# Optimization experiments

Hardware: AMD Instinct MI355X
Metric: run time of the kernel (lower is better)

Reference implementation:

```python
import jax, jax.numpy as jnp
import numpy as np

L, H, C, HS, E, K, V, BS = 2, 12, 768, 64, 8, 2, 32000, 1024
B, T = 2, 1024


def layer_norm(x, s, b):
    mu = x.mean(-1, keepdims=True)
    var = ((x - mu) ** 2).mean(-1, keepdims=True)
    return (x - mu) / jnp.sqrt(var + 1e-5) * s + b


def setup_inputs() -> dict:
    key = jax.random.key(0)
    ks = jax.random.split(key, 16)
    def n(k, shape, s=0.02):
        return jax.random.normal(k, shape, dtype=jnp.float32) * s
    return {
        'idx': jax.random.randint(ks[0], (B, T), 0, V),
        'targets': jax.random.randint(ks[1], (B, T), 0, V),
        'tok_emb': n(ks[2], (V, C)),
        'pos_emb': n(ks[3], (BS, C)),
        'ln1_s': jnp.ones((L, C), jnp.float32), 'ln1_b': jnp.zeros((L, C), jnp.float32),
        'wq': n(ks[4], (L, H, C, HS)), 'wk': n(ks[5], (L, H, C, HS)), 'wv': n(ks[6], (L, H, C, HS)),
        'wo': n(ks[7], (L, C, C)), 'bo': jnp.zeros((L, C), jnp.float32),
        'ln2_s': jnp.ones((L, C), jnp.float32), 'ln2_b': jnp.zeros((L, C), jnp.float32),
        'gate_w': n(ks[8], (L, E, C)),
        'w1': n(ks[9], (L, E, 4 * C, C)), 'b1': jnp.zeros((L, E, 4 * C), jnp.float32),
        'w2': n(ks[10], (L, E, C, 4 * C)), 'b2': jnp.zeros((L, E, C), jnp.float32),
        'lm_w': n(ks[11], (V, C)), 'lm_b': jnp.zeros((V,), jnp.float32),
    }


def reference(idx, targets, tok_emb, pos_emb, ln1_s, ln1_b, wq, wk, wv, wo, bo,
              ln2_s, ln2_b, gate_w, w1, b1, w2, b2, lm_w, lm_b):
    Bsz, Tn = idx.shape
    x = tok_emb[idx] + pos_emb[:Tn]                       # [B,T,C]
    mask = jnp.tril(jnp.ones((Tn, Tn), bool))
    for l in range(L):
        # causal multi-head attention (per-head projections, scale = n_embed**-0.5 as in source)
        h = layer_norm(x, ln1_s[l], ln1_b[l])
        q = jnp.einsum('btc,hcd->bhtd', h, wq[l])
        k = jnp.einsum('btc,hcd->bhtd', h, wk[l])
        v = jnp.einsum('btc,hcd->bhtd', h, wv[l])
        att = jnp.einsum('bhtd,bhsd->bhts', q, k) * (C ** -0.5)
        att = jax.nn.softmax(jnp.where(mask, att, -jnp.inf), axis=-1)
        o = jnp.einsum('bhts,bhsd->bhtd', att, v)
        o = o.transpose(0, 2, 1, 3).reshape(Bsz, Tn, C)   # concat heads
        x = x + jnp.einsum('btc,oc->bto', o, wo[l]) + bo[l]
        # MoE FFN: top-k routing, softmax over selected gate logits
        h2 = layer_norm(x, ln2_s[l], ln2_b[l]).reshape(-1, C)     # [N,C]
        gl = jnp.einsum('tc,ec->te', h2, gate_w[l])               # [N,E]
        wts, sel = jax.lax.top_k(gl, K)
        wts = jax.nn.softmax(wts, axis=-1)
        comb = jnp.einsum('tk,tke->te', wts, jax.nn.one_hot(sel, E, dtype=wts.dtype))
        hid = jax.nn.relu(jnp.einsum('tc,efc->etf', h2, w1[l]) + b1[l][:, None, :])
        y = jnp.einsum('etf,ecf->etc', hid, w2[l]) + b2[l][:, None, :]
        moe = jnp.einsum('te,etc->tc', comb, y)                   # dispatch-weighted combine
        x = x + moe.reshape(Bsz, Tn, C)
    logits = jnp.einsum('btc,vc->btv', x, lm_w) + lm_b
    lf = logits.reshape(-1, V)
    tf = targets.reshape(-1)
    loss = -jnp.take_along_axis(jax.nn.log_softmax(lf, axis=-1), tf[:, None], axis=1).mean()
    return lf, loss
```

## Files before the change

### kernel.cpp

```cpp
#include <hip/hip_runtime.h>
#include <hip/hip_bf16.h>

#define LCNT 2
#define HCNT 12
#define CDIM 768
#define HSD  64
#define ECNT 8
#define VOC  32000
#define BB   2
#define TT   1024
#define NTOK 2048
#define FF   3072
#define QKVLD 2304
#define TOTCAP 5120
#define SKN  4

typedef __attribute__((ext_vector_type(8))) short bf16x8;
typedef __attribute__((ext_vector_type(4))) float f32x4;

__device__ __forceinline__ float wave_sum(float v) {
    #pragma unroll
    for (int off = 32; off; off >>= 1) v += __shfl_xor(v, off);
    return v;
}
__device__ __forceinline__ float wave_max(float v) {
    #pragma unroll
    for (int off = 32; off; off >>= 1) v = fmaxf(v, __shfl_xor(v, off));
    return v;
}
__device__ __forceinline__ unsigned short f2bf(float f) {
    unsigned int u = __float_as_uint(f);
    unsigned int r = (u + 0x7FFFu + ((u >> 16) & 1u)) >> 16;
    return (unsigned short)r;
}
__device__ __forceinline__ float bf2f(unsigned short h) {
    return __uint_as_float((unsigned int)h << 16);
}
__device__ __forceinline__ void split2(float a, unsigned short& h, unsigned short& l) {
    h = f2bf(a);
    l = f2bf(a - bf2f(h));
}
__device__ __forceinline__ ushort4 cvt4(float4 v) {
    ushort4 r;
    r.x = f2bf(v.x); r.y = f2bf(v.y); r.z = f2bf(v.z); r.w = f2bf(v.w);
    return r;
}
__device__ __forceinline__ void gload16(const void* g, void* l) {
    __builtin_amdgcn_global_load_lds(
        (const __attribute__((address_space(1))) unsigned int*)g,
        (__attribute__((address_space(3))) unsigned int*)l,
        16, 0, 0);
}

__global__ __launch_bounds__(256)
void cvt_bf16_kernel(const float* __restrict__ in, unsigned short* __restrict__ out, int n4)
{
    for (int i = blockIdx.x * 256 + threadIdx.x; i < n4; i += gridDim.x * 256) {
        float4 v = reinterpret_cast<const float4*>(in)[i];
        reinterpret_cast<ushort4*>(out)[i] = cvt4(v);
    }
}

__global__ __launch_bounds__(256)
void splitw_kernel(const float* __restrict__ in, unsigned short* __restrict__ oh,
                   unsigned short* __restrict__ ol, int n4)
{
    for (int i = blockIdx.x * 256 + threadIdx.x; i < n4; i += gridDim.x * 256) {
        float4 v = reinterpret_cast<const float4*>(in)[i];
        ushort4 h, l;
        split2(v.x, h.x, l.x); split2(v.y, h.y, l.y);
        split2(v.z, h.z, l.z); split2(v.w, h.w, l.w);
        reinterpret_cast<ushort4*>(oh)[i] = h;
        reinterpret_cast<ushort4*>(ol)[i] = l;
    }
}

__global__ __launch_bounds__(256)
void embed_kernel(const int* __restrict__ idx, const float* __restrict__ tok,
                  const float* __restrict__ pos, float* __restrict__ x)
{
    int i = blockIdx.x * 256 + threadIdx.x;
    int c = i % CDIM;
    int n = i / CDIM;
    int t = n % TT;
    x[i] = tok[(size_t)idx[n] * CDIM + c] + pos[(size_t)t * CDIM + c];
}

__global__ __launch_bounds__(256)
void repack_kernel(const float* __restrict__ wq, const float* __restrict__ wk,
                   const float* __restrict__ wv, unsigned short* __restrict__ wph,
                   unsigned short* __restrict__ wpl)
{
    int i = blockIdx.x * 256 + threadIdx.x;
    int kk = i % CDIM;
    int n  = (i / CDIM) % CDIM;
    int w3 = (i / (CDIM * CDIM)) % 3;
    int l  = i / (CDIM * CDIM * 3);
    const float* src = (w3 == 0) ? wq : (w3 == 1) ? wk : wv;
    int h = n / HSD, d = n % HSD;
    float v = src[((((size_t)l * HCNT + h) * CDIM) + kk) * HSD + d];
    unsigned short hh, ll;
    split2(v, hh, ll);
    size_t o = (((size_t)l * 3 + w3) * CDIM + n) * CDIM + kk;
    wph[o] = hh;
    wpl[o] = ll;
}

__global__ __launch_bounds__(256)
void ln_kernel(const float* __restrict__ x, const float* __restrict__ sc,
               const float* __restrict__ bs, float* __restrict__ out)
{
    int row = blockIdx.x;
    const float* xr = x + (size_t)row * CDIM;
    float* orow = out + (size_t)row * CDIM;
    int tid = threadIdx.x;
    float v0 = xr[tid], v1 = xr[tid + 256], v2 = xr[tid + 512];
    float s1 = v0 + v1 + v2;
    float s2 = v0 * v0 + v1 * v1 + v2 * v2;
    s1 = wave_sum(s1);
    s2 = wave_sum(s2);
    __shared__ float r1[4], r2[4];
    int w = tid >> 6, lane = tid & 63;
    if (lane == 0) { r1[w] = s1; r2[w] = s2; }
    __syncthreads();
    float t1 = r1[0] + r1[1] + r1[2] + r1[3];
    float t2 = r2[0] + r2[1] + r2[2] + r2[3];
    float mu = t1 * (1.0f / CDIM);
    float var = t2 * (1.0f / CDIM) - mu * mu;
    float rstd = rsqrtf(var + 1e-5f);
    orow[tid]       = (v0 - mu) * rstd * sc[tid]       + bs[tid];
    orow[tid + 256] = (v1 - mu) * rstd * sc[tid + 256] + bs[tid + 256];
    orow[tid + 512] = (v2 - mu) * rstd * sc[tid + 512] + bs[tid + 512];
}

#define BM 128
#define BN 128
#define BK 32
#define PADK 40

template<int MODE, bool SPLIT>
__global__ __launch_bounds__(256)
void gemm_bf16_kernel(int Kd,
                      const float* __restrict__ A, int lda,
                      const float* __restrict__ B, int ldb,
                      const float* __restrict__ bias,
                      float* __restrict__ out, int ldo,
                      const int* __restrict__ rowmeta,
                      size_t bstride, int biasstride)
{
    __shared__ short Ah[BM * PADK];
    __shared__ short Bh[BN * PADK];
    __shared__ short Al[SPLIT ? BM * PADK : 2];
    __shared__ short Bl[SPLIT ? BN * PADK : 2];

    int roff = 0;
    if (rowmeta) {
        const int ee = blockIdx.z;
        const int rcnt = rowmeta[2 * ee + 1];
        if ((int)(blockIdx.y * BM) >= rcnt) return;
        roff = rowmeta[2 * ee];
        B += (size_t)ee * bstride;
        if (bias) bias += (size_t)ee * biasstride;
    }

    const int tid = threadIdx.x;
    const int m0 = roff + blockIdx.y * BM;
    const int n0 = blockIdx.x * BN;
    const int w = tid >> 6, lane = tid & 63;
    const int wr = w >> 1, wc = w & 1;
    const int lrow = lane & 15, lkg = lane >> 4;
    const int srow = tid >> 3, skg = (tid & 7) * 4;

    const float* Ablk = A + (size_t)m0 * lda;
    const float* Bblk = B + (size_t)n0 * ldb;

    float4 pa[4], pb[4];
    #pragma unroll
    for (int p = 0; p < 4; ++p) {
        pa[p] = *(const float4*)(Ablk + (size_t)(p * 32 + srow) * lda + skg);
        pb[p] = *(const float4*)(Bblk + (size_t)(p * 32 + srow) * ldb + skg);
    }

    f32x4 acc[4][4] = {};
    const int nk = Kd / BK;

    for (int t = 0; t < nk; ++t) {
        __syncthreads();
        #pragma unroll
        for (int p = 0; p < 4; ++p) {
            if constexpr (SPLIT) {
                ushort4 h, l;
                split2(pa[p].x, h.x, l.x); split2(pa[p].y, h.y, l.y);
                split2(pa[p].z, h.z, l.z); split2(pa[p].w, h.w, l.w);
                *(ushort4*)(&Ah[(p * 32 + srow) * PADK + skg]) = h;
                *(ushort4*)(&Al[(p * 32 + srow) * PADK + skg]) = l;
                split2(pb[p].x, h.x, l.x); split2(pb[p].y, h.y, l.y);
                split2(pb[p].z, h.z, l.z); split2(pb[p].w, h.w, l.w);
                *(ushort4*)(&Bh[(p * 32 + srow) * PADK + skg]) = h;
                *(ushort4*)(&Bl[(p * 32 + srow) * PADK + skg]) = l;
            } else {
                *(ushort4*)(&Ah[(p * 32 + srow) * PADK + skg]) = cvt4(pa[p]);
                *(ushort4*)(&Bh[(p * 32 + srow) * PADK + skg]) = cvt4(pb[p]);
            }
        }
        __syncthreads();
        if (t + 1 < nk) {
            const int kb = (t + 1) * BK + skg;
            #pragma unroll
            for (int p = 0; p < 4; ++p) {
                pa[p] = *(const float4*)(Ablk + (size_t)(p * 32 + srow) * lda + kb);
                pb[p] = *(const float4*)(Bblk + (size_t)(p * 32 + srow) * ldb + kb);
            }
        }
        bf16x8 afh[4], afl[4];
        #pragma unroll
        for (int i = 0; i < 4; ++i) {
            afh[i] = *(const bf16x8*)(&Ah[(wr * 64 + i * 16 + lrow) * PADK + lkg * 8]);
            if constexpr (SPLIT)
                afl[i] = *(const bf16x8*)(&Al[(wr * 64 + i * 16 + lrow) * PADK + lkg * 8]);
        }
        #pragma unroll
        for (int j = 0; j < 4; ++j) {
            const bf16x8 bh = *(const bf16x8*)(&Bh[(wc * 64 + j * 16 + lrow) * PADK + lkg * 8]);
            if constexpr (SPLIT) {
                const bf16x8 bl = *(const bf16x8*)(&Bl[(wc * 64 + j * 16 + lrow) * PADK + lkg * 8]);
                #pragma unroll
                for (int i = 0; i < 4; ++i) {
                    acc[i][j] = __builtin_amdgcn_mfma_f32_16x16x32_bf16(afh[i], bh, acc[i][j], 0, 0, 0);
                    acc[i][j] = __builtin_amdgcn_mfma_f32_16x16x32_bf16(afl[i], bh, acc[i][j], 0, 0, 0);
                    acc[i][j] = __builtin_amdgcn_mfma_f32_16x16x32_bf16(afh[i], bl, acc[i][j], 0, 0, 0);
                }
            } else {
                #pragma unroll
                for (int i = 0; i < 4; ++i)
                    acc[i][j] = __builtin_amdgcn_mfma_f32_16x16x32_bf16(afh[i], bh, acc[i][j], 0, 0, 0);
            }
        }
    }

    #pragma unroll
    for (int i = 0; i < 4; ++i) {
        #pragma unroll
        for (int r = 0; r < 4; ++r) {
            const int row = m0 + wr * 64 + i * 16 + lkg * 4 + r;
            #pragma unroll
            for (int j = 0; j < 4; ++j) {
                const int col = n0 + wc * 64 + j * 16 + lrow;
                const float bj = bias ? bias[col] : 0.0f;
                const float vres = acc[i][j][r] + bj;
                float* op = out + (size_t)row * ldo + col;
                if (MODE == 0) *op = vres;
                else if (MODE == 1) *op = *op + vres;
                else *op = fmaxf(vres, 0.0f);
            }
        }
    }
}

__global__ __launch_bounds__(256)
void gemm_sk_kernel(int Kc,
                    const float* __restrict__ A, int lda,
                    const float* __restrict__ B, int ldb,
                    const float* __restrict__ bias,
                    float* __restrict__ part, int ldo, size_t pstride,
                    const int* __restrict__ rowmeta,
                    size_t bstride, int biasstride)
{
    __shared__ short Ah[BM * PADK];
    __shared__ short Bh[BN * PADK];
    __shared__ short Al[BM * PADK];
    __shared__ short Bl[BN * PADK];

    const int zz = blockIdx.z;
    const int ee = zz / SKN, kz = zz % SKN;
    const int rcnt = rowmeta[2 * ee + 1];
    if ((int)(blockIdx.y * BM) >= rcnt) return;
    const int roff = rowmeta[2 * ee];
    const float* Bp = B + (size_t)ee * bstride + (size_t)kz * Kc;
    const float* Ap = A + (size_t)kz * Kc;
    const float* biasp = (kz == 0 && bias) ? bias + (size_t)ee * biasstride : nullptr;
    float* out = part + (size_t)kz * pstride;

    const int tid = threadIdx.x;
    const int m0 = roff + blockIdx.y * BM;
    const int n0 = blockIdx.x * BN;
    const int w = tid >> 6, lane = tid & 63;
    const int wr = w >> 1, wc = w & 1;
    const int lrow = lane & 15, lkg = lane >> 4;
    const int srow = tid >> 3, skg = (tid & 7) * 4;

    const float* Ablk = Ap + (size_t)m0 * lda;
    const float* Bblk = Bp + (size_t)n0 * ldb;

    float4 pa[4], pb[4];
    #pragma unroll
    for (int p = 0; p < 4; ++p) {
        pa[p] = *(const float4*)(Ablk + (size_t)(p * 32 + srow) * lda + skg);
        pb[p] = *(const float4*)(Bblk + (size_t)(p * 32 + srow) * ldb + skg);
    }

    f32x4 acc[4][4] = {};
    const int nk = Kc / BK;

    for (int t = 0; t < nk; ++t) {
        __syncthreads();
        #pragma unroll
        for (int p = 0; p < 4; ++p) {
            ushort4 h, l;
            split2(pa[p].x, h.x, l.x); split2(pa[p].y, h.y, l.y);
            split2(pa[p].z, h.z, l.z); split2(pa[p].w, h.w, l.w);
            *(ushort4*)(&Ah[(p * 32 + srow) * PADK + skg]) = h;
            *(ushort4*)(&Al[(p * 32 + srow) * PADK + skg]) = l;
            split2(pb[p].x, h.x, l.x); split2(pb[p].y, h.y, l.y);
            split2(pb[p].z, h.z, l.z); split2(pb[p].w, h.w, l.w);
            *(ushort4*)(&Bh[(p * 32 + srow) * PADK + skg]) = h;
            *(ushort4*)(&Bl[(p * 32 + srow) * PADK + skg]) = l;
        }
        __syncthreads();
        if (t + 1 < nk) {
            const int kb = (t + 1) * BK + skg;
            #pragma unroll
            for (int p = 0; p < 4; ++p) {
                pa[p] = *(const float4*)(Ablk + (size_t)(p * 32 + srow) * lda + kb);
                pb[p] = *(const float4*)(Bblk + (size_t)(p * 32 + srow) * ldb + kb);
            }
        }
        bf16x8 afh[4], afl[4];
        #pragma unroll
        for (int i = 0; i < 4; ++i) {
            afh[i] = *(const bf16x8*)(&Ah[(wr * 64 + i * 16 + lrow) * PADK + lkg * 8]);
            afl[i] = *(const bf16x8*)(&Al[(wr * 64 + i * 16 + lrow) * PADK + lkg * 8]);
        }
        #pragma unroll
        for (int j = 0; j < 4; ++j) {
            const bf16x8 bh = *(const bf16x8*)(&Bh[(wc * 64 + j * 16 + lrow) * PADK + lkg * 8]);
            const bf16x8 bl = *(const bf16x8*)(&Bl[(wc * 64 + j * 16 + lrow) * PADK + lkg * 8]);
            #pragma unroll
            for (int i = 0; i < 4; ++i) {
                acc[i][j] = __builtin_amdgcn_mfma_f32_16x16x32_bf16(afh[i], bh, acc[i][j], 0, 0, 0);
                acc[i][j] = __builtin_amdgcn_mfma_f32_16x16x32_bf16(afl[i], bh, acc[i][j], 0, 0, 0);
                acc[i][j] = __builtin_amdgcn_mfma_f32_16x16x32_bf16(afh[i], bl, acc[i][j], 0, 0, 0);
            }
        }
    }

    #pragma unroll
    for (int i = 0; i < 4; ++i) {
        #pragma unroll
        for (int r = 0; r < 4; ++r) {
            const int row = m0 + wr * 64 + i * 16 + lkg * 4 + r;
            #pragma unroll
            for (int j = 0; j < 4; ++j) {
                const int col = n0 + wc * 64 + j * 16 + lrow;
                const float bj = biasp ? biasp[col] : 0.0f;
                out[(size_t)row * ldo + col] = acc[i][j][r] + bj;
            }
        }
    }
}

template<int MODE, bool OUTSPLIT>
__global__ __launch_bounds__(256)
void gemm_splitpb_kernel(int Kd,
                         const float* __restrict__ A, int lda,
                         const unsigned short* __restrict__ Bhg,
                         const unsigned short* __restrict__ Blg, int ldb,
                         const float* __restrict__ bias,
                         float* __restrict__ out,
                         unsigned short* __restrict__ outh,
                         unsigned short* __restrict__ outl, int ldo)
{
    __shared__ short Ah[BM * PADK];
    __shared__ short Al[BM * PADK];
    __shared__ short Bh[BN * PADK];
    __shared__ short Bl[BN * PADK];

    const int tid = threadIdx.x;
    const int m0 = blockIdx.y * BM;
    const int n0 = blockIdx.x * BN;
    const int w = tid >> 6, lane = tid & 63;
    const int wr = w >> 1, wc = w & 1;
    const int lrow = lane & 15, lkg = lane >> 4;
    const int srow = tid >> 3, skg = (tid & 7) * 4;

    const float* Ablk = A + (size_t)m0 * lda;
    const unsigned short* Bhblk = Bhg + (size_t)n0 * ldb;
    const unsigned short* Blblk = Blg + (size_t)n0 * ldb;

    float4 pa[4];
    ushort4 pbh[4], pbl[4];
    #pragma unroll
    for (int p = 0; p < 4; ++p) {
        pa[p]  = *(const float4*)(Ablk + (size_t)(p * 32 + srow) * lda + skg);
        pbh[p] = *(const ushort4*)(Bhblk + (size_t)(p * 32 + srow) * ldb + skg);
        pbl[p] = *(const ushort4*)(Blblk + (size_t)(p * 32 + srow) * ldb + skg);
    }

    f32x4 acc[4][4] = {};
    const int nk = Kd / BK;

    for (int t = 0; t < nk; ++t) {
        __syncthreads();
        #pragma unroll
        for (int p = 0; p < 4; ++p) {
            ushort4 h, l;
            split2(pa[p].x, h.x, l.x); split2(pa[p].y, h.y, l.y);
            split2(pa[p].z, h.z, l.z); split2(pa[p].w, h.w, l.w);
            *(ushort4*)(&Ah[(p * 32 + srow) * PADK + skg]) = h;
            *(ushort4*)(&Al[(p * 32 + srow) * PADK + skg]) = l;
            *(ushort4*)(&Bh[(p * 32 + srow) * PADK + skg]) = pbh[p];
            *(ushort4*)(&Bl[(p * 32 + srow) * PADK + skg]) = pbl[p];
        }
        __syncthreads();
        if (t + 1 < nk) {
            const int kb = (t + 1) * BK + skg;
            #pragma unroll
            for (int p = 0; p < 4; ++p) {
                pa[p]  = *(const float4*)(Ablk + (size_t)(p * 32 + srow) * lda + kb);
                pbh[p] = *(const ushort4*)(Bhblk + (size_t)(p * 32 + srow) * ldb + kb);
                pbl[p] = *(const ushort4*)(Blblk + (size_t)(p * 32 + srow) * ldb + kb);
            }
        }
        bf16x8 afh[4], afl[4];
        #pragma unroll
        for (int i = 0; i < 4; ++i) {
            afh[i] = *(const bf16x8*)(&Ah[(wr * 64 + i * 16 + lrow) * PADK + lkg * 8]);
            afl[i] = *(const bf16x8*)(&Al[(wr * 64 + i * 16 + lrow) * PADK + lkg * 8]);
        }
        #pragma unroll
        for (int j = 0; j < 4; ++j) {
            const bf16x8 bh = *(const bf16x8*)(&Bh[(wc * 64 + j * 16 + lrow) * PADK + lkg * 8]);
            const bf16x8 bl = *(const bf16x8*)(&Bl[(wc * 64 + j * 16 + lrow) * PADK + lkg * 8]);
            #pragma unroll
            for (int i = 0; i < 4; ++i) {
                acc[i][j] = __builtin_amdgcn_mfma_f32_16x16x32_bf16(afh[i], bh, acc[i][j], 0, 0, 0);
                acc[i][j] = __builtin_amdgcn_mfma_f32_16x16x32_bf16(afl[i], bh, acc[i][j], 0, 0, 0);
                acc[i][j] = __builtin_amdgcn_mfma_f32_16x16x32_bf16(afh[i], bl, acc[i][j], 0, 0, 0);
            }
        }
    }

    #pragma unroll
    for (int i = 0; i < 4; ++i) {
        #pragma unroll
        for (int r = 0; r < 4; ++r) {
            const int row = m0 + wr * 64 + i * 16 + lkg * 4 + r;
            #pragma unroll
            for (int j = 0; j < 4; ++j) {
                const int col = n0 + wc * 64 + j * 16 + lrow;
                const float bj = bias ? bias[col] : 0.0f;
                const float vres = acc[i][j][r] + bj;
                if constexpr (OUTSPLIT) {
                    unsigned short h, l;
                    split2(vres, h, l);
                    outh[(size_t)row * ldo + col] = h;
                    outl[(size_t)row * ldo + col] = l;
                } else {
                    float* op = out + (size_t)row * ldo + col;
                    if (MODE == 0) *op = vres;
                    else *op = *op + vres;
                }
            }
        }
    }
}

template<int MODE, bool SWZ, bool OUTBF, bool BBF>
__global__ __launch_bounds__(256)
void gemm_fastw_kernel(int Kd,
                       const unsigned short* __restrict__ A, int lda,
                       const void* __restrict__ Bv, int ldb,
                       const float* __restrict__ bias,
                       void* __restrict__ outv, int ldo,
                       const int* __restrict__ rowmeta,
                       size_t bstride, int biasstride)
{
    __shared__ short Ah[BM * PADK];
    __shared__ short Bh[BN * PADK];

    int bx = blockIdx.x, by = blockIdx.y;
    if constexpr (SWZ) {
        const int nwg = gridDim.x * gridDim.y;
        const int chunk = nwg >> 3;
        const int flat = by * gridDim.x + bx;
        const int newid = (flat & 7) * chunk + (flat >> 3);
        by = newid % gridDim.y;
        bx = newid / gridDim.y;
    }

    const float* Bf = (const float*)Bv;
    const unsigned short* Bb = (const unsigned short*)Bv;
    float* outf = (float*)outv;
    unsigned short* outb = (unsigned short*)outv;

    int roff = 0;
    if (rowmeta) {
        const int ee = blockIdx.z;
        const int rcnt = rowmeta[2 * ee + 1];
        if ((int)(by * BM) >= rcnt) return;
        roff = rowmeta[2 * ee];
        if (BBF) Bb += (size_t)ee * bstride; else Bf += (size_t)ee * bstride;
        if (bias) bias += (size_t)ee * biasstride;
    }

    const int tid = threadIdx.x;
    const int m0 = roff + by * BM;
    const int n0 = bx * BN;
    const int w = tid >> 6, lane = tid & 63;
    const int wr = w >> 1, wc = w & 1;
    const int lrow = lane & 15, lkg = lane >> 4;
    const int srow = tid >> 3, skg = (tid & 7) * 4;

    const unsigned short* Ablk = A + (size_t)m0 * lda;
    const float* Bfblk = Bf + (size_t)n0 * ldb;
    const unsigned short* Bbblk = Bb + (size_t)n0 * ldb;

    ushort4 pa[4];
    ushort4 pbb[4];
    float4  pbf[4];
    #pragma unroll
    for (int p = 0; p < 4; ++p) {
        pa[p] = *(const ushort4*)(Ablk + (size_t)(p * 32 + srow) * lda + skg);
        if constexpr (BBF) pbb[p] = *(const ushort4*)(Bbblk + (size_t)(p * 32 + srow) * ldb + skg);
        else               pbf[p] = *(const float4*)(Bfblk + (size_t)(p * 32 + srow) * ldb + skg);
    }

    f32x4 acc[4][4] = {};
    const int nk = Kd / BK;

    for (int t = 0; t < nk; ++t) {
        __syncthreads();
        #pragma unroll
        for (int p = 0; p < 4; ++p) {
            *(ushort4*)(&Ah[(p * 32 + srow) * PADK + skg]) = pa[p];
            *(ushort4*)(&Bh[(p * 32 + srow) * PADK + skg]) = BBF ? pbb[p] : cvt4(pbf[p]);
        }
        __syncthreads();
        if (t + 1 < nk) {
            const int kb = (t + 1) * BK + skg;
            #pragma unroll
            for (int p = 0; p < 4; ++p) {
                pa[p] = *(const ushort4*)(Ablk + (size_t)(p * 32 + srow) * lda + kb);
                if constexpr (BBF) pbb[p] = *(const ushort4*)(Bbblk + (size_t)(p * 32 + srow) * ldb + kb);
                else               pbf[p] = *(const float4*)(Bfblk + (size_t)(p * 32 + srow) * ldb + kb);
            }
        }
        bf16x8 af[4];
        #pragma unroll
        for (int i = 0; i < 4; ++i)
            af[i] = *(const bf16x8*)(&Ah[(wr * 64 + i * 16 + lrow) * PADK + lkg * 8]);
        #pragma unroll
        for (int j = 0; j < 4; ++j) {
            const bf16x8 bh = *(const bf16x8*)(&Bh[(wc * 64 + j * 16 + lrow) * PADK + lkg * 8]);
            #pragma unroll
            for (int i = 0; i < 4; ++i)
                acc[i][j] = __builtin_amdgcn_mfma_f32_16x16x32_bf16(af[i], bh, acc[i][j], 0, 0, 0);
        }
    }

    #pragma unroll
    for (int i = 0; i < 4; ++i) {
        #pragma unroll
        for (int r = 0; r < 4; ++r) {
            const int row = m0 + wr * 64 + i * 16 + lkg * 4 + r;
            #pragma unroll
            for (int j = 0; j < 4; ++j) {
                const int col = n0 + wc * 64 + j * 16 + lrow;
                const float bj = bias ? bias[col] : 0.0f;
                float vres = acc[i][j][r] + bj;
                if (MODE == 2) vres = fmaxf(vres, 0.0f);
                if constexpr (OUTBF) outb[(size_t)row * ldo + col] = f2bf(vres);
                else                 outf[(size_t)row * ldo + col] = vres;
            }
        }
    }
}

template<bool SWZ>
__global__ __launch_bounds__(256)
void gemm_lds_kernel(int Kd,
                     const unsigned short* __restrict__ A, int lda,
                     const unsigned short* __restrict__ B, int ldb,
                     const float* __restrict__ bias,
                     float* __restrict__ out, int ldo)
{
    __shared__ unsigned short Asl[BM * BK];
    __shared__ unsigned short Bsl[BN * BK];

    int bx = blockIdx.x, by = blockIdx.y;
    if constexpr (SWZ) {
        const int nwg = gridDim.x * gridDim.y;
        const int chunk = nwg >> 3;
        const int flat = by * gridDim.x + bx;
        const int newid = (flat & 7) * chunk + (flat >> 3);
        by = newid % gridDim.y;
        bx = newid / gridDim.y;
    }

    const int tid = threadIdx.x;
    const int m0 = by * BM;
    const int n0 = bx * BN;
    const int w = tid >> 6, lane = tid & 63;
    const int wr = w >> 1, wc = w & 1;
    const int lrow = lane & 15, lkg = lane >> 4;
    const int grow = lane >> 2, gcol = (lane & 3) * 8;

    const unsigned short* Ablk = A + (size_t)m0 * lda;
    const unsigned short* Bblk = B + (size_t)n0 * ldb;

    f32x4 acc[4][4] = {};
    const int nk = Kd / BK;

    for (int t = 0; t < nk; ++t) {
        const int k0 = t * BK;
        __syncthreads();
        #pragma unroll
        for (int j = 0; j < 2; ++j) {
            const int rbase = w * 32 + j * 16;
            gload16(Ablk + (size_t)(rbase + grow) * lda + k0 + gcol, Asl + rbase * BK);
            gload16(Bblk + (size_t)(rbase + grow) * ldb + k0 + gcol, Bsl + rbase * BK);
        }
        __syncthreads();

        bf16x8 af[4];
        #pragma unroll
        for (int i = 0; i < 4; ++i)
            af[i] = *(const bf16x8*)(Asl + (wr * 64 + i * 16 + lrow) * BK + lkg * 8);
        #pragma unroll
        for (int j = 0; j < 4; ++j) {
            const bf16x8 bh = *(const bf16x8*)(Bsl + (wc * 64 + j * 16 + lrow) * BK + lkg * 8);
            #pragma unroll
            for (int i = 0; i < 4; ++i)
                acc[i][j] = __builtin_amdgcn_mfma_f32_16x16x32_bf16(af[i], bh, acc[i][j], 0, 0, 0);
        }
    }

    #pragma unroll
    for (int i = 0; i < 4; ++i) {
        #pragma unroll
        for (int r = 0; r < 4; ++r) {
            const int row = m0 + wr * 64 + i * 16 + lkg * 4 + r;
            #pragma unroll
            for (int j = 0; j < 4; ++j) {
                const int col = n0 + wc * 64 + j * 16 + lrow;
                const float bj = bias ? bias[col] : 0.0f;
                out[(size_t)row * ldo + col] = acc[i][j][r] + bj;
            }
        }
    }
}

#define QBLK 64
#define KVBLK 64

__global__ __launch_bounds__(256)
void attn_mfma_kernel(const unsigned short* __restrict__ qh_g,
                      const unsigned short* __restrict__ ql_g,
                      float* __restrict__ o)
{
    __shared__ short Kh[2][KVBLK][PADK];
    __shared__ short Kl[2][KVBLK][PADK];
    __shared__ short Vh[2][HSD][PADK];
    __shared__ short Vl[2][HSD][PADK];
    __shared__ short Ph[4][2][16][PADK];
    __shared__ short Pl[4][2][16][PADK];

    const int t0 = blockIdx.x * QBLK;
    const int bh = blockIdx.y;
    const int b = bh / HCNT, hh = bh % HCNT;
    const size_t baseq = (size_t)b * TT * QKVLD + (size_t)hh * HSD;
    const size_t obase = (size_t)b * TT * CDIM + (size_t)hh * HSD;
    const unsigned short* kh_g = qh_g + baseq + CDIM;
    const unsigned short* kl_g = ql_g + baseq + CDIM;
    const unsigned short* vh_g = qh_g + baseq + 2 * CDIM;
    const unsigned short* vl_g = ql_g + baseq + 2 * CDIM;
    const int tid = threadIdx.x;
    const int w = tid >> 6, lane = tid & 63;
    const int lrow = lane & 15, lkg = lane >> 4;
    const float sscale = rsqrtf((float)CDIM);

    bf16x8 qh[2], ql[2];
    {
        const size_t qroff = baseq + (size_t)(t0 + w * 16 + lrow) * QKVLD;
        #pragma unroll
        for (int ks = 0; ks < 2; ++ks) {
            qh[ks] = *(const bf16x8*)(qh_g + qroff + ks * 32 + lkg * 8);
            ql[ks] = *(const bf16x8*)(ql_g + qroff + ks * 32 + lkg * 8);
        }
    }

    f32x4 oacc[4] = {};
    float m_[4], l_[4];
    #pragma unroll
    for (int rr = 0; rr < 4; ++rr) { m_[rr] = -1e30f; l_[rr] = 0.0f; }

    for (int s0 = 0; s0 <= t0 + QBLK - 1; s0 += KVBLK) {
        __syncthreads();
        {
            const int srow = tid >> 3, skg = (tid & 7) * 4;
            #pragma unroll
            for (int p = 0; p < 2; ++p) {
                const size_t kroff = (size_t)(s0 + p * 32 + srow) * QKVLD;
                #pragma unroll
                for (int ks = 0; ks < 2; ++ks) {
                    *(ushort4*)(&Kh[ks][p * 32 + srow][skg]) = *(const ushort4*)(kh_g + kroff + ks * 32 + skg);
                    *(ushort4*)(&Kl[ks][p * 32 + srow][skg]) = *(const ushort4*)(kl_g + kroff + ks * 32 + skg);
                }
            }
            const int key = tid & 63, dg = (tid >> 6) * 16;
            const size_t vroff = (size_t)(s0 + key) * QKVLD + dg;
            const int kst = key >> 5, ko = key & 31;
            #pragma unroll
            for (int dd = 0; dd < 16; dd += 4) {
                ushort4 hv = *(const ushort4*)(vh_g + vroff + dd);
                ushort4 lv = *(const ushort4*)(vl_g + vroff + dd);
                Vh[kst][dg + dd + 0][ko] = hv.x; Vl[kst][dg + dd + 0][ko] = lv.x;
                Vh[kst][dg + dd + 1][ko] = hv.y; Vl[kst][dg + dd + 1][ko] = lv.y;
                Vh[kst][dg + dd + 2][ko] = hv.z; Vl[kst][dg + dd + 2][ko] = lv.z;
                Vh[kst][dg + dd + 3][ko] = hv.w; Vl[kst][dg + dd + 3][ko] = lv.w;
            }
        }
        __syncthreads();

        f32x4 sacc[4] = {};
        #pragma unroll
        for (int j = 0; j < 4; ++j) {
            #pragma unroll
            for (int ks = 0; ks < 2; ++ks) {
                const bf16x8 bh = *(const bf16x8*)(&Kh[ks][j * 16 + lrow][lkg * 8]);
                const bf16x8 bl = *(const bf16x8*)(&Kl[ks][j * 16 + lrow][lkg * 8]);
                sacc[j] = __builtin_amdgcn_mfma_f32_16x16x32_bf16(qh[ks], bh, sacc[j], 0, 0, 0);
                sacc[j] = __builtin_amdgcn_mfma_f32_16x16x32_bf16(ql[ks], bh, sacc[j], 0, 0, 0);
                sacc[j] = __builtin_amdgcn_mfma_f32_16x16x32_bf16(qh[ks], bl, sacc[j], 0, 0, 0);
            }
        }

        #pragma unroll
        for (int rr = 0; rr < 4; ++rr) {
            const int qi = t0 + w * 16 + lkg * 4 + rr;
            float pv[4];
            float mx = -1e30f;
            #pragma unroll
            for (int j = 0; j < 4; ++j) {
                float s = sacc[j][rr] * sscale;
                if (s0 + j * 16 + lrow > qi) s = -1e30f;
                pv[j] = s;
                mx = fmaxf(mx, s);
            }
            #pragma unroll
            for (int off = 1; off < 16; off <<= 1) mx = fmaxf(mx, __shfl_xor(mx, off));
            const float mnew = fmaxf(m_[rr], mx);
            const float corr = __expf(m_[rr] - mnew);
            float ps = 0.0f;
            #pragma unroll
            for (int j = 0; j < 4; ++j) { pv[j] = __expf(pv[j] - mnew); ps += pv[j]; }
            #pragma unroll
            for (int off = 1; off < 16; off <<= 1) ps += __shfl_xor(ps, off);
            l_[rr] = l_[rr] * corr + ps;
            m_[rr] = mnew;
            #pragma unroll
            for (int jd = 0; jd < 4; ++jd) oacc[jd][rr] *= corr;
            #pragma unroll
            for (int j = 0; j < 4; ++j) {
                unsigned short h, l;
                split2(pv[j], h, l);
                const int key = j * 16 + lrow;
                Ph[w][key >> 5][lkg * 4 + rr][key & 31] = h;
                Pl[w][key >> 5][lkg * 4 + rr][key & 31] = l;
            }
        }

        #pragma unroll
        for (int ks = 0; ks < 2; ++ks) {
            const bf16x8 ah = *(const bf16x8*)(&Ph[w][ks][lrow][lkg * 8]);
            const bf16x8 al = *(const bf16x8*)(&Pl[w][ks][lrow][lkg * 8]);
            #pragma unroll
            for (int jd = 0; jd < 4; ++jd) {
                const bf16x8 bh = *(const bf16x8*)(&Vh[ks][jd * 16 + lrow][lkg * 8]);
                const bf16x8 bl = *(const bf16x8*)(&Vl[ks][jd * 16 + lrow][lkg * 8]);
                oacc[jd] = __builtin_amdgcn_mfma_f32_16x16x32_bf16(ah, bh, oacc[jd], 0, 0, 0);
                oacc[jd] = __builtin_amdgcn_mfma_f32_16x16x32_bf16(al, bh, oacc[jd], 0, 0, 0);
                oacc[jd] = __builtin_amdgcn_mfma_f32_16x16x32_bf16(ah, bl, oacc[jd], 0, 0, 0);
            }
        }
    }

    #pragma unroll
    for (int rr = 0; rr < 4; ++rr) {
        const int qi = t0 + w * 16 + lkg * 4 + rr;
        const float invl = 1.0f / l_[rr];
        float* orow = o + obase + (size_t)qi * CDIM;
        #pragma unroll
        for (int jd = 0; jd < 4; ++jd)
            orow[jd * 16 + lrow] = oacc[jd][rr] * invl;
    }
}

__global__ __launch_bounds__(256)
void gate_kernel(const float* __restrict__ h2, const float* __restrict__ gw,
                 int2* __restrict__ sel, float2* __restrict__ wts)
{
    __shared__ float gws[ECNT * CDIM];
    int tid = threadIdx.x;
    for (int i = tid; i < ECNT * CDIM; i += 256) gws[i] = gw[i];
    __syncthreads();
    int t = blockIdx.x * 256 + tid;
    const float* hr = h2 + (size_t)t * CDIM;
    float g[ECNT] = {};
    for (int c = 0; c < CDIM; ++c) {
        float hv = hr[c];
        #pragma unroll
        for (int e = 0; e < ECNT; ++e) g[e] = fmaf(hv, gws[e * CDIM + c], g[e]);
    }
    int e0 = 0; float g0 = g[0];
    #pragma unroll
    for (int e = 1; e < ECNT; ++e) if (g[e] > g0) { g0 = g[e]; e0 = e; }
    int e1 = -1; float g1 = -1e30f;
    #pragma unroll
    for (int e = 0; e < ECNT; ++e) if (e != e0 && g[e] > g1) { g1 = g[e]; e1 = e; }
    float z = __expf(g1 - g0);
    float w0 = 1.0f / (1.0f + z);
    sel[t] = make_int2(e0, e1);
    wts[t] = make_float2(w0, 1.0f - w0);
}

__global__ __launch_bounds__(256)
void route_kernel(const int2* __restrict__ sel, int* __restrict__ perm,
                  int* __restrict__ tokpos, int* __restrict__ meta)
{
    __shared__ int cnt[ECNT], off[ECNT], cur[ECNT];
    const int tid = threadIdx.x;
    if (tid < ECNT) cnt[tid] = 0;
    __syncthreads();
    for (int t = tid; t < NTOK; t += 256) {
        atomicAdd(&cnt[sel[t].x], 1);
        atomicAdd(&cnt[sel[t].y], 1);
    }
    __syncthreads();
    if (tid == 0) {
        int run = 0;
        for (int e = 0; e < ECNT; ++e) {
            off[e] = run; cur[e] = 0;
            int pc = (cnt[e] + BM - 1) / BM * BM;
            meta[2 * e] = run; meta[2 * e + 1] = pc;
            run += pc;
        }
    }
    __syncthreads();
    for (int p = tid; p < TOTCAP; p += 256) perm[p] = 0;
    __syncthreads();
    for (int t = tid; t < NTOK; t += 256) {
        int2 s = sel[t];
        int p0 = atomicAdd(&cur[s.x], 1); perm[off[s.x] + p0] = t; tokpos[2 * t]     = off[s.x] + p0;
        int p1 = atomicAdd(&cur[s.y], 1); perm[off[s.y] + p1] = t; tokpos[2 * t + 1] = off[s.y] + p1;
    }
}

__global__ __launch_bounds__(256)
void gather_kernel(const float* __restrict__ h2, const int* __restrict__ perm,
                   float* __restrict__ xg)
{
    int i = blockIdx.x * 256 + threadIdx.x;
    int c = i % CDIM, p = i / CDIM;
    xg[i] = h2[(size_t)perm[p] * CDIM + c];
}

__global__ __launch_bounds__(256)
void gather_bf16_kernel(const float* __restrict__ h2, const int* __restrict__ perm,
                        unsigned short* __restrict__ xg)
{
    int i = blockIdx.x * 256 + threadIdx.x;
    int c = i % CDIM, p = i / CDIM;
    xg[i] = f2bf(h2[(size_t)perm[p] * CDIM + c]);
}

template<int SK>
__global__ __launch_bounds__(256)
void combine_kernel(const float* __restrict__ y, size_t pstride,
                    const int* __restrict__ tokpos,
                    const float2* __restrict__ wts, float* __restrict__ x)
{
    int i = blockIdx.x * 256 + threadIdx.x;
    int c = i % CDIM, t = i / CDIM;
    float2 wv = wts[t];
    const size_t r0 = (size_t)tokpos[2 * t] * CDIM + c;
    const size_t r1 = (size_t)tokpos[2 * t + 1] * CDIM + c;
    float a0 = 0.0f, a1 = 0.0f;
    #pragma unroll
    for (int s = 0; s < SK; ++s) {
        a0 += y[s * pstride + r0];
        a1 += y[s * pstride + r1];
    }
    x[i] += wv.x * a0 + wv.y * a1;
}

__global__ __launch_bounds__(256)
void loss_row_kernel(const float* __restrict__ logits, const int* __restrict__ tgt,
                     float* __restrict__ lrow)
{
    int row = blockIdx.x;
    const float* lr = logits + (size_t)row * VOC;
    int tid = threadIdx.x, w = tid >> 6, lane = tid & 63;
    __shared__ float red[4];
    float mx = -1e30f;
    for (int i = tid; i < VOC; i += 256) mx = fmaxf(mx, lr[i]);
    mx = wave_max(mx);
    if (lane == 0) red[w] = mx;
    __syncthreads();
    mx = fmaxf(fmaxf(red[0], red[1]), fmaxf(red[2], red[3]));
    __syncthreads();
    float se = 0.0f;
    for (int i = tid; i < VOC; i += 256) se += expf(lr[i] - mx);
    se = wave_sum(se);
    if (lane == 0) red[w] = se;
    __syncthreads();
    if (tid == 0) {
        float lse = mx + logf(red[0] + red[1] + red[2] + red[3]);
        lrow[row] = lse - lr[tgt[row]];
    }
}

__global__ __launch_bounds__(256)
void loss_reduce_kernel(const float* __restrict__ lrow, float* __restrict__ out)
{
    int tid = threadIdx.x, w = tid >> 6, lane = tid & 63;
    float s = 0.0f;
    for (int i = tid; i < NTOK; i += 256) s += lrow[i];
    s = wave_sum(s);
    __shared__ float red[4];
    if (lane == 0) red[w] = s;
    __syncthreads();
    if (tid == 0) out[0] = (red[0] + red[1] + red[2] + red[3]) * (1.0f / NTOK);
}

extern "C" void kernel_launch(void* const* d_in, const int* in_sizes, int n_in,
                              void* d_out, int out_size, void* d_ws, size_t ws_size,
                              hipStream_t stream)
{
    const int*   idx     = (const int*)d_in[0];
    const int*   targets = (const int*)d_in[1];
    const float* tok_emb = (const float*)d_in[2];
    const float* pos_emb = (const float*)d_in[3];
    const float* ln1_s   = (const float*)d_in[4];
    const float* ln1_b   = (const float*)d_in[5];
    const float* wq      = (const float*)d_in[6];
    const float* wk      = (const float*)d_in[7];
    const float* wv      = (const float*)d_in[8];
    const float* wo      = (const float*)d_in[9];
    const float* bo      = (const float*)d_in[10];
    const float* ln2_s   = (const float*)d_in[11];
    const float* ln2_b   = (const float*)d_in[12];
    const float* gate_w  = (const float*)d_in[13];
    const float* w1      = (const float*)d_in[14];
    const float* b1      = (const float*)d_in[15];
    const float* w2      = (const float*)d_in[16];
    const float* b2      = (const float*)d_in[17];
    const float* lm_w    = (const float*)d_in[18];
    const float* lm_b    = (const float*)d_in[19];
    float* out = (float*)d_out;

    unsigned short* wph = (unsigned short*)d_ws;
    unsigned short* wpl = wph + (size_t)3 * LCNT * CDIM * CDIM;
    unsigned short* woh = wpl + (size_t)3 * LCNT * CDIM * CDIM;
    unsigned short* wol = woh + (size_t)LCNT * CDIM * CDIM;
    float* x    = (float*)(wol + (size_t)LCNT * CDIM * CDIM);
    float* hbuf = x    + (size_t)NTOK * CDIM;
    float* qkv  = hbuf + (size_t)NTOK * CDIM;
    float* xg   = qkv  + (size_t)NTOK * QKVLD;
    float* hid  = xg   + (size_t)TOTCAP * CDIM;
    float* lrow = hid  + (size_t)TOTCAP * FF;
    float2* wts = (float2*)(lrow + NTOK);
    int2*  sel  = (int2*)(wts + NTOK);
    int*   perm = (int*)(sel + NTOK);
    int*  tokpos= perm + TOTCAP;
    int*   meta = tokpos + 2 * NTOK;
    unsigned short* x_bf = (unsigned short*)(meta + 16);
    float* part = (float*)(x_bf + (size_t)NTOK * CDIM);

    const size_t need_bytes = (size_t)((char*)(part + (size_t)SKN * TOTCAP * CDIM) - (char*)d_ws);
    const bool use_sk = ws_size >= need_bytes;

    unsigned short* qkvh = (unsigned short*)qkv;
    unsigned short* qkvl = qkvh + (size_t)NTOK * QKVLD;
    unsigned short* xg_bf  = (unsigned short*)xg;
    unsigned short* hid_bf = (unsigned short*)hid;
    unsigned short* lmw_bf = (unsigned short*)hid;

    dim3 blk(256);

    repack_kernel<<<(3 * LCNT * CDIM * CDIM) / 256, blk, 0, stream>>>(wq, wk, wv, wph, wpl);
    splitw_kernel<<<1024, blk, 0, stream>>>(wo, woh, wol, LCNT * CDIM * CDIM / 4);
    embed_kernel<<<(NTOK * CDIM) / 256, blk, 0, stream>>>(idx, tok_emb, pos_emb, x);

    for (int l = 0; l < LCNT; ++l) {
        ln_kernel<<<NTOK, blk, 0, stream>>>(x, ln1_s + (size_t)l * CDIM, ln1_b + (size_t)l * CDIM, hbuf);

        gemm_splitpb_kernel<0, true><<<dim3(QKVLD / BN, NTOK / BM), blk, 0, stream>>>(
            CDIM, hbuf, CDIM, wph + (size_t)l * 3 * CDIM * CDIM, wpl + (size_t)l * 3 * CDIM * CDIM,
            CDIM, nullptr, nullptr, qkvh, qkvl, QKVLD);

        attn_mfma_kernel<<<dim3(TT / QBLK, BB * HCNT), blk, 0, stream>>>(qkvh, qkvl, hbuf);

        gemm_splitpb_kernel<1, false><<<dim3(CDIM / BN, NTOK / BM), blk, 0, stream>>>(
            CDIM, hbuf, CDIM, woh + (size_t)l * CDIM * CDIM, wol + (size_t)l * CDIM * CDIM,
            CDIM, bo + (size_t)l * CDIM, x, nullptr, nullptr, CDIM);

        float* h2 = qkv;
        float* ybuf = qkv;
        ln_kernel<<<NTOK, blk, 0, stream>>>(x, ln2_s + (size_t)l * CDIM, ln2_b + (size_t)l * CDIM, h2);
        gate_kernel<<<NTOK / 256, blk, 0, stream>>>(h2, gate_w + (size_t)l * ECNT * CDIM, sel, wts);
        route_kernel<<<1, blk, 0, stream>>>(sel, perm, tokpos, meta);

        const float* w1l = w1 + (size_t)l * ECNT * FF * CDIM;
        const float* b1l = b1 + (size_t)l * ECNT * FF;
        const float* w2l = w2 + (size_t)l * ECNT * CDIM * FF;
        const float* b2l = b2 + (size_t)l * ECNT * CDIM;
        if (l == 0) {
            gather_kernel<<<(TOTCAP * CDIM) / 256, blk, 0, stream>>>(h2, perm, xg);
            gemm_bf16_kernel<2, true><<<dim3(FF / BN, TOTCAP / BM, ECNT), blk, 0, stream>>>(
                CDIM, xg, CDIM, w1l, CDIM, b1l, hid, FF, meta, (size_t)FF * CDIM, FF);
            if (use_sk) {
                gemm_sk_kernel<<<dim3(CDIM / BN, TOTCAP / BM, ECNT * SKN), blk, 0, stream>>>(
                    FF / SKN, hid, FF, w2l, FF, b2l, part, CDIM, (size_t)TOTCAP * CDIM,
                    meta, (size_t)CDIM * FF, CDIM);
                combine_kernel<SKN><<<(NTOK * CDIM) / 256, blk, 0, stream>>>(
                    part, (size_t)TOTCAP * CDIM, tokpos, wts, x);
            } else {
                gemm_bf16_kernel<0, true><<<dim3(CDIM / BN, TOTCAP / BM, ECNT), blk, 0, stream>>>(
                    FF, hid, FF, w2l, FF, b2l, ybuf, CDIM, meta, (size_t)CDIM * FF, CDIM);
                combine_kernel<1><<<(NTOK * CDIM) / 256, blk, 0, stream>>>(
                    ybuf, 0, tokpos, wts, x);
            }
        } else {
            gather_bf16_kernel<<<(TOTCAP * CDIM) / 256, blk, 0, stream>>>(h2, perm, xg_bf);
            gemm_fastw_kernel<2, false, true, false><<<dim3(FF / BN, TOTCAP / BM, ECNT), blk, 0, stream>>>(
                CDIM, xg_bf, CDIM, w1l, CDIM, b1l, hid_bf, FF, meta, (size_t)FF * CDIM, FF);
            gemm_fastw_kernel<0, false, false, false><<<dim3(CDIM / BN, TOTCAP / BM, ECNT), blk, 0, stream>>>(
                FF, hid_bf, FF, w2l, FF, b2l, ybuf, CDIM, meta, (size_t)CDIM * FF, CDIM);
            combine_kernel<1><<<(NTOK * CDIM) / 256, blk, 0, stream>>>(
                ybuf, 0, tokpos, wts, x);
        }
    }

    cvt_bf16_kernel<<<2048, blk, 0, stream>>>(lm_w, lmw_bf, VOC * CDIM / 4);
    cvt_bf16_kernel<<<512, blk, 0, stream>>>(x, x_bf, NTOK * CDIM / 4);

    gemm_lds_kernel<true><<<dim3(VOC / BN, NTOK / BM), blk, 0, stream>>>(
        CDIM, x_bf, CDIM, lmw_bf, CDIM, lm_b, out, VOC);

    loss_row_kernel<<<NTOK, blk, 0, stream>>>(out, targets, lrow);
    loss_reduce_kernel<<<1, blk, 0, stream>>>(lrow, out + (size_t)NTOK * VOC);
}
```

Before: 1.372 ms.

## Pre-split activations into bf16 hi/lo pairs at producers instead of in GEMMs

LayerNorm, attention output and the first MoE GEMM now write activations as separate bf16 high/low halves. Consumer GEMMs load those halves directly instead of loading fp32 and splitting each tile inside the K loop. This removes repeated split arithmetic and halves nothing in bytes (hi+lo equals fp32 size), but moves the conversion out of the hot loop and lets gathers copy shorts. The loss row kernel is also vectorised with float4 loads.

```diff
diff --git a/kernel.cpp b/kernel.cpp
--- a/kernel.cpp
+++ b/kernel.cpp
@@ -106,13 +106,14 @@
     wpl[o] = ll;
 }
 
+template<bool WF32>
 __global__ __launch_bounds__(256)
 void ln_kernel(const float* __restrict__ x, const float* __restrict__ sc,
-               const float* __restrict__ bs, float* __restrict__ out)
+               const float* __restrict__ bs, float* __restrict__ out,
+               unsigned short* __restrict__ oh, unsigned short* __restrict__ ol)
 {
     int row = blockIdx.x;
     const float* xr = x + (size_t)row * CDIM;
-    float* orow = out + (size_t)row * CDIM;
     int tid = threadIdx.x;
     float v0 = xr[tid], v1 = xr[tid + 256], v2 = xr[tid + 512];
     float s1 = v0 + v1 + v2;
@@ -128,9 +129,19 @@
     float mu = t1 * (1.0f / CDIM);
     float var = t2 * (1.0f / CDIM) - mu * mu;
     float rstd = rsqrtf(var + 1e-5f);
-    orow[tid]       = (v0 - mu) * rstd * sc[tid]       + bs[tid];
-    orow[tid + 256] = (v1 - mu) * rstd * sc[tid + 256] + bs[tid + 256];
-    orow[tid + 512] = (v2 - mu) * rstd * sc[tid + 512] + bs[tid + 512];
+    float o0 = (v0 - mu) * rstd * sc[tid]       + bs[tid];
+    float o1 = (v1 - mu) * rstd * sc[tid + 256] + bs[tid + 256];
+    float o2 = (v2 - mu) * rstd * sc[tid + 512] + bs[tid + 512];
+    if constexpr (WF32) {
+        float* orow = out + (size_t)row * CDIM;
+        orow[tid] = o0; orow[tid + 256] = o1; orow[tid + 512] = o2;
+    }
+    unsigned short h, l;
+    unsigned short* ohr = oh + (size_t)row * CDIM;
+    unsigned short* olr = ol + (size_t)row * CDIM;
+    split2(o0, h, l); ohr[tid]       = h; olr[tid]       = l;
+    split2(o1, h, l); ohr[tid + 256] = h; olr[tid + 256] = l;
+    split2(o2, h, l); ohr[tid + 512] = h; olr[tid + 512] = l;
 }
 
 #define BM 128
@@ -138,237 +149,17 @@
 #define BK 32
 #define PADK 40
 
-template<int MODE, bool SPLIT>
-__global__ __launch_bounds__(256)
-void gemm_bf16_kernel(int Kd,
-                      const float* __restrict__ A, int lda,
-                      const float* __restrict__ B, int ldb,
-                      const float* __restrict__ bias,
-                      float* __restrict__ out, int ldo,
-                      const int* __restrict__ rowmeta,
-                      size_t bstride, int biasstride)
-{
-    __shared__ short Ah[BM * PADK];
-    __shared__ short Bh[BN * PADK];
-    __shared__ short Al[SPLIT ? BM * PADK : 2];
-    __shared__ short Bl[SPLIT ? BN * PADK : 2];
-
-    int roff = 0;
-    if (rowmeta) {
-        const int ee = blockIdx.z;
-        const int rcnt = rowmeta[2 * ee + 1];
-        if ((int)(blockIdx.y * BM) >= rcnt) return;
-        roff = rowmeta[2 * ee];
-        B += (size_t)ee * bstride;
-        if (bias) bias += (size_t)ee * biasstride;
-    }
-
-    const int tid = threadIdx.x;
-    const int m0 = roff + blockIdx.y * BM;
-    const int n0 = blockIdx.x * BN;
-    const int w = tid >> 6, lane = tid & 63;
-    const int wr = w >> 1, wc = w & 1;
-    const int lrow = lane & 15, lkg = lane >> 4;
-    const int srow = tid >> 3, skg = (tid & 7) * 4;
-
-    const float* Ablk = A + (size_t)m0 * lda;
-    const float* Bblk = B + (size_t)n0 * ldb;
-
-    float4 pa[4], pb[4];
-    #pragma unroll
-    for (int p = 0; p < 4; ++p) {
-        pa[p] = *(const float4*)(Ablk + (size_t)(p * 32 + srow) * lda + skg);
-        pb[p] = *(const float4*)(Bblk + (size_t)(p * 32 + srow) * ldb + skg);
-    }
-
-    f32x4 acc[4][4] = {};
-    const int nk = Kd / BK;
-
-    for (int t = 0; t < nk; ++t) {
-        __syncthreads();
-        #pragma unroll
-        for (int p = 0; p < 4; ++p) {
-            if constexpr (SPLIT) {
-                ushort4 h, l;
-                split2(pa[p].x, h.x, l.x); split2(pa[p].y, h.y, l.y);
-                split2(pa[p].z, h.z, l.z); split2(pa[p].w, h.w, l.w);
-                *(ushort4*)(&Ah[(p * 32 + srow) * PADK + skg]) = h;
-                *(ushort4*)(&Al[(p * 32 + srow) * PADK + skg]) = l;
-                split2(pb[p].x, h.x, l.x); split2(pb[p].y, h.y, l.y);
-                split2(pb[p].z, h.z, l.z); split2(pb[p].w, h.w, l.w);
-                *(ushort4*)(&Bh[(p * 32 + srow) * PADK + skg]) = h;
-                *(ushort4*)(&Bl[(p * 32 + srow) * PADK + skg]) = l;
-            } else {
-                *(ushort4*)(&Ah[(p * 32 + srow) * PADK + skg]) = cvt4(pa[p]);
-                *(ushort4*)(&Bh[(p * 32 + srow) * PADK + skg]) = cvt4(pb[p]);
-            }
-        }
-        __syncthreads();
-        if (t + 1 < nk) {
-            const int kb = (t + 1) * BK + skg;
-            #pragma unroll
-            for (int p = 0; p < 4; ++p) {
-                pa[p] = *(const float4*)(Ablk + (size_t)(p * 32 + srow) * lda + kb);
-                pb[p] = *(const float4*)(Bblk + (size_t)(p * 32 + srow) * ldb + kb);
-            }
-        }
-        bf16x8 afh[4], afl[4];
-        #pragma unroll
-        for (int i = 0; i < 4; ++i) {
-            afh[i] = *(const bf16x8*)(&Ah[(wr * 64 + i * 16 + lrow) * PADK + lkg * 8]);
-            if constexpr (SPLIT)
-                afl[i] = *(const bf16x8*)(&Al[(wr * 64 + i * 16 + lrow) * PADK + lkg * 8]);
-        }
-        #pragma unroll
-        for (int j = 0; j < 4; ++j) {
-            const bf16x8 bh = *(const bf16x8*)(&Bh[(wc * 64 + j * 16 + lrow) * PADK + lkg * 8]);
-            if constexpr (SPLIT) {
-                const bf16x8 bl = *(const bf16x8*)(&Bl[(wc * 64 + j * 16 + lrow) * PADK + lkg * 8]);
-                #pragma unroll
-                for (int i = 0; i < 4; ++i) {
-                    acc[i][j] = __builtin_amdgcn_mfma_f32_16x16x32_bf16(afh[i], bh, acc[i][j], 0, 0, 0);
-                    acc[i][j] = __builtin_amdgcn_mfma_f32_16x16x32_bf16(afl[i], bh, acc[i][j], 0, 0, 0);
-                    acc[i][j] = __builtin_amdgcn_mfma_f32_16x16x32_bf16(afh[i], bl, acc[i][j], 0, 0, 0);
-                }
-            } else {
-                #pragma unroll
-                for (int i = 0; i < 4; ++i)
-                    acc[i][j] = __builtin_amdgcn_mfma_f32_16x16x32_bf16(afh[i], bh, acc[i][j], 0, 0, 0);
-            }
-        }
-    }
-
-    #pragma unroll
-    for (int i = 0; i < 4; ++i) {
-        #pragma unroll
-        for (int r = 0; r < 4; ++r) {
-            const int row = m0 + wr * 64 + i * 16 + lkg * 4 + r;
-            #pragma unroll
-            for (int j = 0; j < 4; ++j) {
-                const int col = n0 + wc * 64 + j * 16 + lrow;
-                const float bj = bias ? bias[col] : 0.0f;
-                const float vres = acc[i][j][r] + bj;
-                float* op = out + (size_t)row * ldo + col;
-                if (MODE == 0) *op = vres;
-                else if (MODE == 1) *op = *op + vres;
-                else *op = fmaxf(vres, 0.0f);
-            }
-        }
-    }
-}
-
-__global__ __launch_bounds__(256)
-void gemm_sk_kernel(int Kc,
-                    const float* __restrict__ A, int lda,
-                    const float* __restrict__ B, int ldb,
+template<int MODE, bool OUTSPLIT>
+__global__ __launch_bounds__(256)
+void gemm_ps_kernel(int Kd,
+                    const unsigned short* __restrict__ Ahg,
+                    const unsigned short* __restrict__ Alg, int lda,
+                    const unsigned short* __restrict__ Bhg,
+                    const unsigned short* __restrict__ Blg, int ldb,
                     const float* __restrict__ bias,
-                    float* __restrict__ part, int ldo, size_t pstride,
-                    const int* __restrict__ rowmeta,
-                    size_t bstride, int biasstride)
-{
-    __shared__ short Ah[BM * PADK];
-    __shared__ short Bh[BN * PADK];
-    __shared__ short Al[BM * PADK];
-    __shared__ short Bl[BN * PADK];
-
-    const int zz = blockIdx.z;
-    const int ee = zz / SKN, kz = zz % SKN;
-    const int rcnt = rowmeta[2 * ee + 1];
-    if ((int)(blockIdx.y * BM) >= rcnt) return;
-    const int roff = rowmeta[2 * ee];
-    const float* Bp = B + (size_t)ee * bstride + (size_t)kz * Kc;
-    const float* Ap = A + (size_t)kz * Kc;
-    const float* biasp = (kz == 0 && bias) ? bias + (size_t)ee * biasstride : nullptr;
-    float* out = part + (size_t)kz * pstride;
-
-    const int tid = threadIdx.x;
-    const int m0 = roff + blockIdx.y * BM;
-    const int n0 = blockIdx.x * BN;
-    const int w = tid >> 6, lane = tid & 63;
-    const int wr = w >> 1, wc = w & 1;
-    const int lrow = lane & 15, lkg = lane >> 4;
-    const int srow = tid >> 3, skg = (tid & 7) * 4;
-
-    const float* Ablk = Ap + (size_t)m0 * lda;
-    const float* Bblk = Bp + (size_t)n0 * ldb;
-
-    float4 pa[4], pb[4];
-    #pragma unroll
-    for (int p = 0; p < 4; ++p) {
-        pa[p] = *(const float4*)(Ablk + (size_t)(p * 32 + srow) * lda + skg);
-        pb[p] = *(const float4*)(Bblk + (size_t)(p * 32 + srow) * ldb + skg);
-    }
-
-    f32x4 acc[4][4] = {};
-    const int nk = Kc / BK;
-
-    for (int t = 0; t < nk; ++t) {
-        __syncthreads();
-        #pragma unroll
-        for (int p = 0; p < 4; ++p) {
-            ushort4 h, l;
-            split2(pa[p].x, h.x, l.x); split2(pa[p].y, h.y, l.y);
-            split2(pa[p].z, h.z, l.z); split2(pa[p].w, h.w, l.w);
-            *(ushort4*)(&Ah[(p * 32 + srow) * PADK + skg]) = h;
-            *(ushort4*)(&Al[(p * 32 + srow) * PADK + skg]) = l;
-            split2(pb[p].x, h.x, l.x); split2(pb[p].y, h.y, l.y);
-            split2(pb[p].z, h.z, l.z); split2(pb[p].w, h.w, l.w);
-            *(ushort4*)(&Bh[(p * 32 + srow) * PADK + skg]) = h;
-            *(ushort4*)(&Bl[(p * 32 + srow) * PADK + skg]) = l;
-        }
-        __syncthreads();
-        if (t + 1 < nk) {
-            const int kb = (t + 1) * BK + skg;
-            #pragma unroll
-            for (int p = 0; p < 4; ++p) {
-                pa[p] = *(const float4*)(Ablk + (size_t)(p * 32 + srow) * lda + kb);
-                pb[p] = *(const float4*)(Bblk + (size_t)(p * 32 + srow) * ldb + kb);
-            }
-        }
-        bf16x8 afh[4], afl[4];
-        #pragma unroll
-        for (int i = 0; i < 4; ++i) {
-            afh[i] = *(const bf16x8*)(&Ah[(wr * 64 + i * 16 + lrow) * PADK + lkg * 8]);
-            afl[i] = *(const bf16x8*)(&Al[(wr * 64 + i * 16 + lrow) * PADK + lkg * 8]);
-        }
-        #pragma unroll
-        for (int j = 0; j < 4; ++j) {
-            const bf16x8 bh = *(const bf16x8*)(&Bh[(wc * 64 + j * 16 + lrow) * PADK + lkg * 8]);
-            const bf16x8 bl = *(const bf16x8*)(&Bl[(wc * 64 + j * 16 + lrow) * PADK + lkg * 8]);
-            #pragma unroll
-            for (int i = 0; i < 4; ++i) {
-                acc[i][j] = __builtin_amdgcn_mfma_f32_16x16x32_bf16(afh[i], bh, acc[i][j], 0, 0, 0);
-                acc[i][j] = __builtin_amdgcn_mfma_f32_16x16x32_bf16(afl[i], bh, acc[i][j], 0, 0, 0);
-                acc[i][j] = __builtin_amdgcn_mfma_f32_16x16x32_bf16(afh[i], bl, acc[i][j], 0, 0, 0);
-            }
-        }
-    }
-
-    #pragma unroll
-    for (int i = 0; i < 4; ++i) {
-        #pragma unroll
-        for (int r = 0; r < 4; ++r) {
-            const int row = m0 + wr * 64 + i * 16 + lkg * 4 + r;
-            #pragma unroll
-            for (int j = 0; j < 4; ++j) {
-                const int col = n0 + wc * 64 + j * 16 + lrow;
-                const float bj = biasp ? biasp[col] : 0.0f;
-                out[(size_t)row * ldo + col] = acc[i][j][r] + bj;
-            }
-        }
-    }
-}
-
-template<int MODE, bool OUTSPLIT>
-__global__ __launch_bounds__(256)
-void gemm_splitpb_kernel(int Kd,
-                         const float* __restrict__ A, int lda,
-                         const unsigned short* __restrict__ Bhg,
-                         const unsigned short* __restrict__ Blg, int ldb,
-                         const float* __restrict__ bias,
-                         float* __restrict__ out,
-                         unsigned short* __restrict__ outh,
-                         unsigned short* __restrict__ outl, int ldo)
+                    float* __restrict__ out,
+                    unsigned short* __restrict__ outh,
+                    unsigned short* __restrict__ outl, int ldo)
 {
     __shared__ short Ah[BM * PADK];
     __shared__ short Al[BM * PADK];
@@ -383,17 +174,18 @@
     const int lrow = lane & 15, lkg = lane >> 4;
     const int srow = tid >> 3, skg = (tid & 7) * 4;
 
-    const float* Ablk = A + (size_t)m0 * lda;
-    const unsigned short* Bhblk = Bhg + (size_t)n0 * ldb;
-    const unsigned short* Blblk = Blg + (size_t)n0 * ldb;
-
-    float4 pa[4];
-    ushort4 pbh[4], pbl[4];
+    const unsigned short* Ahb = Ahg + (size_t)m0 * lda;
+    const unsigned short* Alb = Alg + (size_t)m0 * lda;
+    const unsigned short* Bhb = Bhg + (size_t)n0 * ldb;
+    const unsigned short* Blb = Blg + (size_t)n0 * ldb;
+
+    ushort4 pah[4], pal[4], pbh[4], pbl[4];
     #pragma unroll
     for (int p = 0; p < 4; ++p) {
-        pa[p]  = *(const float4*)(Ablk + (size_t)(p * 32 + srow) * lda + skg);
-        pbh[p] = *(const ushort4*)(Bhblk + (size_t)(p * 32 + srow) * ldb + skg);
-        pbl[p] = *(const ushort4*)(Blblk + (size_t)(p * 32 + srow) * ldb + skg);
+        pah[p] = *(const ushort4*)(Ahb + (size_t)(p * 32 + srow) * lda + skg);
+        pal[p] = *(const ushort4*)(Alb + (size_t)(p * 32 + srow) * lda + skg);
+        pbh[p] = *(const ushort4*)(Bhb + (size_t)(p * 32 + srow) * ldb + skg);
+        pbl[p] = *(const ushort4*)(Blb + (size_t)(p * 32 + srow) * ldb + skg);
     }
 
     f32x4 acc[4][4] = {};
@@ -403,11 +195,8 @@
         __syncthreads();
         #pragma unroll
         for (int p = 0; p < 4; ++p) {
-            ushort4 h, l;
-            split2(pa[p].x, h.x, l.x); split2(pa[p].y, h.y, l.y);
-            split2(pa[p].z, h.z, l.z); split2(pa[p].w, h.w, l.w);
-            *(ushort4*)(&Ah[(p * 32 + srow) * PADK + skg]) = h;
-            *(ushort4*)(&Al[(p * 32 + srow) * PADK + skg]) = l;
+            *(ushort4*)(&Ah[(p * 32 + srow) * PADK + skg]) = pah[p];
+            *(ushort4*)(&Al[(p * 32 + srow) * PADK + skg]) = pal[p];
             *(ushort4*)(&Bh[(p * 32 + srow) * PADK + skg]) = pbh[p];
             *(ushort4*)(&Bl[(p * 32 + srow) * PADK + skg]) = pbl[p];
         }
@@ -416,9 +205,10 @@
             const int kb = (t + 1) * BK + skg;
             #pragma unroll
             for (int p = 0; p < 4; ++p) {
-                pa[p]  = *(const float4*)(Ablk + (size_t)(p * 32 + srow) * lda + kb);
-                pbh[p] = *(const ushort4*)(Bhblk + (size_t)(p * 32 + srow) * ldb + kb);
-                pbl[p] = *(const ushort4*)(Blblk + (size_t)(p * 32 + srow) * ldb + kb);
+                pah[p] = *(const ushort4*)(Ahb + (size_t)(p * 32 + srow) * lda + kb);
+                pal[p] = *(const ushort4*)(Alb + (size_t)(p * 32 + srow) * lda + kb);
+                pbh[p] = *(const ushort4*)(Bhb + (size_t)(p * 32 + srow) * ldb + kb);
+                pbl[p] = *(const ushort4*)(Blb + (size_t)(p * 32 + srow) * ldb + kb);
             }
         }
         bf16x8 afh[4], afl[4];
@@ -465,6 +255,219 @@
     }
 }
 
+__global__ __launch_bounds__(256)
+void gemm_pse_kernel(int Kd,
+                     const unsigned short* __restrict__ Ahg,
+                     const unsigned short* __restrict__ Alg, int lda,
+                     const float* __restrict__ B, int ldb,
+                     const float* __restrict__ bias,
+                     unsigned short* __restrict__ outh,
+                     unsigned short* __restrict__ outl, int ldo,
+                     const int* __restrict__ rowmeta,
+                     size_t bstride, int biasstride)
+{
+    __shared__ short Ah[BM * PADK];
+    __shared__ short Al[BM * PADK];
+    __shared__ short Bh[BN * PADK];
+    __shared__ short Bl[BN * PADK];
+
+    const int ee = blockIdx.z;
+    const int rcnt = rowmeta[2 * ee + 1];
+    if ((int)(blockIdx.y * BM) >= rcnt) return;
+    const int roff = rowmeta[2 * ee];
+    B += (size_t)ee * bstride;
+    bias += (size_t)ee * biasstride;
+
+    const int tid = threadIdx.x;
+    const int m0 = roff + blockIdx.y * BM;
+    const int n0 = blockIdx.x * BN;
+    const int w = tid >> 6, lane = tid & 63;
+    const int wr = w >> 1, wc = w & 1;
+    const int lrow = lane & 15, lkg = lane >> 4;
+    const int srow = tid >> 3, skg = (tid & 7) * 4;
+
+    const unsigned short* Ahb = Ahg + (size_t)m0 * lda;
+    const unsigned short* Alb = Alg + (size_t)m0 * lda;
+    const float* Bblk = B + (size_t)n0 * ldb;
+
+    ushort4 pah[4], pal[4];
+    float4 pb[4];
+    #pragma unroll
+    for (int p = 0; p < 4; ++p) {
+        pah[p] = *(const ushort4*)(Ahb + (size_t)(p * 32 + srow) * lda + skg);
+        pal[p] = *(const ushort4*)(Alb + (size_t)(p * 32 + srow) * lda + skg);
+        pb[p]  = *(const float4*)(Bblk + (size_t)(p * 32 + srow) * ldb + skg);
+    }
+
+    f32x4 acc[4][4] = {};
+    const int nk = Kd / BK;
+
+    for (int t = 0; t < nk; ++t) {
+        __syncthreads();
+        #pragma unroll
+        for (int p = 0; p < 4; ++p) {
+            *(ushort4*)(&Ah[(p * 32 + srow) * PADK + skg]) = pah[p];
+            *(ushort4*)(&Al[(p * 32 + srow) * PADK + skg]) = pal[p];
+            ushort4 h, l;
+            split2(pb[p].x, h.x, l.x); split2(pb[p].y, h.y, l.y);
+            split2(pb[p].z, h.z, l.z); split2(pb[p].w, h.w, l.w);
+            *(ushort4*)(&Bh[(p * 32 + srow) * PADK + skg]) = h;
+            *(ushort4*)(&Bl[(p * 32 + srow) * PADK + skg]) = l;
+        }
+        __syncthreads();
+        if (t + 1 < nk) {
+            const int kb = (t + 1) * BK + skg;
+            #pragma unroll
+            for (int p = 0; p < 4; ++p) {
+                pah[p] = *(const ushort4*)(Ahb + (size_t)(p * 32 + srow) * lda + kb);
+                pal[p] = *(const ushort4*)(Alb + (size_t)(p * 32 + srow) * lda + kb);
+                pb[p]  = *(const float4*)(Bblk + (size_t)(p * 32 + srow) * ldb + kb);
+            }
+        }
+        bf16x8 afh[4], afl[4];
+        #pragma unroll
+        for (int i = 0; i < 4; ++i) {
+            afh[i] = *(const bf16x8*)(&Ah[(wr * 64 + i * 16 + lrow) * PADK + lkg * 8]);
+            afl[i] = *(const bf16x8*)(&Al[(wr * 64 + i * 16 + lrow) * PADK + lkg * 8]);
+        }
+        #pragma unroll
+        for (int j = 0; j < 4; ++j) {
+            const bf16x8 bh = *(const bf16x8*)(&Bh[(wc * 64 + j * 16 + lrow) * PADK + lkg * 8]);
+            const bf16x8 bl = *(const bf16x8*)(&Bl[(wc * 64 + j * 16 + lrow) * PADK + lkg * 8]);
+            #pragma unroll
+            for (int i = 0; i < 4; ++i) {
+                acc[i][j] = __builtin_amdgcn_mfma_f32_16x16x32_bf16(afh[i], bh, acc[i][j], 0, 0, 0);
+                acc[i][j] = __builtin_amdgcn_mfma_f32_16x16x32_bf16(afl[i], bh, acc[i][j], 0, 0, 0);
+                acc[i][j] = __builtin_amdgcn_mfma_f32_16x16x32_bf16(afh[i], bl, acc[i][j], 0, 0, 0);
+            }
+        }
+    }
+
+    #pragma unroll
+    for (int i = 0; i < 4; ++i) {
+        #pragma unroll
+        for (int r = 0; r < 4; ++r) {
+            const int row = m0 + wr * 64 + i * 16 + lkg * 4 + r;
+            #pragma unroll
+            for (int j = 0; j < 4; ++j) {
+                const int col = n0 + wc * 64 + j * 16 + lrow;
+                const float vres = fmaxf(acc[i][j][r] + bias[col], 0.0f);
+                unsigned short h, l;
+                split2(vres, h, l);
+                outh[(size_t)row * ldo + col] = h;
+                outl[(size_t)row * ldo + col] = l;
+            }
+        }
+    }
+}
+
+template<int SK>
+__global__ __launch_bounds__(256)
+void gemm_pssk_kernel(int Kc,
+                      const unsigned short* __restrict__ Ahg,
+                      const unsigned short* __restrict__ Alg, int lda,
+                      const float* __restrict__ B, int ldb,
+                      const float* __restrict__ bias,
+                      float* __restrict__ part, int ldo, size_t pstride,
+                      const int* __restrict__ rowmeta,
+                      size_t bstride, int biasstride)
+{
+    __shared__ short Ah[BM * PADK];
+    __shared__ short Al[BM * PADK];
+    __shared__ short Bh[BN * PADK];
+    __shared__ short Bl[BN * PADK];
+
+    const int zz = blockIdx.z;
+    const int ee = zz / SK, kz = zz % SK;
+    const int rcnt = rowmeta[2 * ee + 1];
+    if ((int)(blockIdx.y * BM) >= rcnt) return;
+    const int roff = rowmeta[2 * ee];
+    const float* Bp = B + (size_t)ee * bstride + (size_t)kz * Kc;
+    const unsigned short* Ahp = Ahg + (size_t)kz * Kc;
+    const unsigned short* Alp = Alg + (size_t)kz * Kc;
+    const float* biasp = (kz == 0) ? bias + (size_t)ee * biasstride : nullptr;
+    float* out = part + (size_t)kz * pstride;
+
+    const int tid = threadIdx.x;
+    const int m0 = roff + blockIdx.y * BM;
+    const int n0 = blockIdx.x * BN;
+    const int w = tid >> 6, lane = tid & 63;
+    const int wr = w >> 1, wc = w & 1;
+    const int lrow = lane & 15, lkg = lane >> 4;
+    const int srow = tid >> 3, skg = (tid & 7) * 4;
+
+    const unsigned short* Ahb = Ahp + (size_t)m0 * lda;
+    const unsigned short* Alb = Alp + (size_t)m0 * lda;
+    const float* Bblk = Bp + (size_t)n0 * ldb;
+
+    ushort4 pah[4], pal[4];
+    float4 pb[4];
+    #pragma unroll
+    for (int p = 0; p < 4; ++p) {
+        pah[p] = *(const ushort4*)(Ahb + (size_t)(p * 32 + srow) * lda + skg);
+        pal[p] = *(const ushort4*)(Alb + (size_t)(p * 32 + srow) * lda + skg);
+        pb[p]  = *(const float4*)(Bblk + (size_t)(p * 32 + srow) * ldb + skg);
+    }
+
+    f32x4 acc[4][4] = {};
+    const int nk = Kc / BK;
+
+    for (int t = 0; t < nk; ++t) {
+        __syncthreads();
+        #pragma unroll
+        for (int p = 0; p < 4; ++p) {
+            *(ushort4*)(&Ah[(p * 32 + srow) * PADK + skg]) = pah[p];
+            *(ushort4*)(&Al[(p * 32 + srow) * PADK + skg]) = pal[p];
+            ushort4 h, l;
+            split2(pb[p].x, h.x, l.x); split2(pb[p].y, h.y, l.y);
+            split2(pb[p].z, h.z, l.z); split2(pb[p].w, h.w, l.w);
+            *(ushort4*)(&Bh[(p * 32 + srow) * PADK + skg]) = h;
+            *(ushort4*)(&Bl[(p * 32 + srow) * PADK + skg]) = l;
+        }
+        __syncthreads();
+        if (t + 1 < nk) {
+            const int kb = (t + 1) * BK + skg;
+            #pragma unroll
+            for (int p = 0; p < 4; ++p) {
+                pah[p] = *(const ushort4*)(Ahb + (size_t)(p * 32 + srow) * lda + kb);
+                pal[p] = *(const ushort4*)(Alb + (size_t)(p * 32 + srow) * lda + kb);
+                pb[p]  = *(const float4*)(Bblk + (size_t)(p * 32 + srow) * ldb + kb);
+            }
+        }
+        bf16x8 afh[4], afl[4];
+        #pragma unroll
+        for (int i = 0; i < 4; ++i) {
+            afh[i] = *(const bf16x8*)(&Ah[(wr * 64 + i * 16 + lrow) * PADK + lkg * 8]);
+            afl[i] = *(const bf16x8*)(&Al[(wr * 64 + i * 16 + lrow) * PADK + lkg * 8]);
+        }
+        #pragma unroll
+        for (int j = 0; j < 4; ++j) {
+            const bf16x8 bh = *(const bf16x8*)(&Bh[(wc * 64 + j * 16 + lrow) * PADK + lkg * 8]);
+            const bf16x8 bl = *(const bf16x8*)(&Bl[(wc * 64 + j * 16 + lrow) * PADK + lkg * 8]);
+            #pragma unroll
+            for (int i = 0; i < 4; ++i) {
+                acc[i][j] = __builtin_amdgcn_mfma_f32_16x16x32_bf16(afh[i], bh, acc[i][j], 0, 0, 0);
+                acc[i][j] = __builtin_amdgcn_mfma_f32_16x16x32_bf16(afl[i], bh, acc[i][j], 0, 0, 0);
+                acc[i][j] = __builtin_amdgcn_mfma_f32_16x16x32_bf16(afh[i], bl, acc[i][j], 0, 0, 0);
+            }
+        }
+    }
+
+    #pragma unroll
+    for (int i = 0; i < 4; ++i) {
+        #pragma unroll
+        for (int r = 0; r < 4; ++r) {
+            const int row = m0 + wr * 64 + i * 16 + lkg * 4 + r;
+            #pragma unroll
+            for (int j = 0; j < 4; ++j) {
+                const int col = n0 + wc * 64 + j * 16 + lrow;
+                const float bj = biasp ? biasp[col] : 0.0f;
+                out[(size_t)row * ldo + col] = acc[i][j][r] + bj;
+            }
+        }
+    }
+}
+
 template<int MODE, bool SWZ, bool OUTBF, bool BBF>
 __global__ __launch_bounds__(256)
 void gemm_fastw_kernel(int Kd,
@@ -656,7 +659,8 @@
 __global__ __launch_bounds__(256)
 void attn_mfma_kernel(const unsigned short* __restrict__ qh_g,
                       const unsigned short* __restrict__ ql_g,
-                      float* __restrict__ o)
+                      unsigned short* __restrict__ oh_g,
+                      unsigned short* __restrict__ ol_g)
 {
     __shared__ short Kh[2][KVBLK][PADK];
     __shared__ short Kl[2][KVBLK][PADK];
@@ -789,10 +793,14 @@
     for (int rr = 0; rr < 4; ++rr) {
         const int qi = t0 + w * 16 + lkg * 4 + rr;
         const float invl = 1.0f / l_[rr];
-        float* orow = o + obase + (size_t)qi * CDIM;
-        #pragma unroll
-        for (int jd = 0; jd < 4; ++jd)
-            orow[jd * 16 + lrow] = oacc[jd][rr] * invl;
+        const size_t orow = obase + (size_t)qi * CDIM;
+        #pragma unroll
+        for (int jd = 0; jd < 4; ++jd) {
+            unsigned short h, l;
+            split2(oacc[jd][rr] * invl, h, l);
+            oh_g[orow + jd * 16 + lrow] = h;
+            ol_g[orow + jd * 16 + lrow] = l;
+        }
     }
 }
 
@@ -857,21 +865,26 @@
 }
 
 __global__ __launch_bounds__(256)
-void gather_kernel(const float* __restrict__ h2, const int* __restrict__ perm,
-                   float* __restrict__ xg)
+void gather_ps_kernel(const unsigned short* __restrict__ h2h,
+                      const unsigned short* __restrict__ h2l,
+                      const int* __restrict__ perm,
+                      unsigned short* __restrict__ xgh,
+                      unsigned short* __restrict__ xgl)
 {
     int i = blockIdx.x * 256 + threadIdx.x;
     int c = i % CDIM, p = i / CDIM;
-    xg[i] = h2[(size_t)perm[p] * CDIM + c];
-}
-
-__global__ __launch_bounds__(256)
-void gather_bf16_kernel(const float* __restrict__ h2, const int* __restrict__ perm,
-                        unsigned short* __restrict__ xg)
+    const size_t s = (size_t)perm[p] * CDIM + c;
+    xgh[i] = h2h[s];
+    xgl[i] = h2l[s];
+}
+
+__global__ __launch_bounds__(256)
+void gather_cp_kernel(const unsigned short* __restrict__ h2h, const int* __restrict__ perm,
+                      unsigned short* __restrict__ xg)
 {
     int i = blockIdx.x * 256 + threadIdx.x;
     int c = i % CDIM, p = i / CDIM;
-    xg[i] = f2bf(h2[(size_t)perm[p] * CDIM + c]);
+    xg[i] = h2h[(size_t)perm[p] * CDIM + c];
 }
 
 template<int SK>
@@ -899,24 +912,30 @@
                      float* __restrict__ lrow)
 {
     int row = blockIdx.x;
-    const float* lr = logits + (size_t)row * VOC;
+    const float4* lr4 = (const float4*)(logits + (size_t)row * VOC);
     int tid = threadIdx.x, w = tid >> 6, lane = tid & 63;
     __shared__ float red[4];
     float mx = -1e30f;
-    for (int i = tid; i < VOC; i += 256) mx = fmaxf(mx, lr[i]);
+    for (int i = tid; i < VOC / 4; i += 256) {
+        float4 v = lr4[i];
+        mx = fmaxf(mx, fmaxf(fmaxf(v.x, v.y), fmaxf(v.z, v.w)));
+    }
     mx = wave_max(mx);
     if (lane == 0) red[w] = mx;
     __syncthreads();
     mx = fmaxf(fmaxf(red[0], red[1]), fmaxf(red[2], red[3]));
     __syncthreads();
     float se = 0.0f;
-    for (int i = tid; i < VOC; i += 256) se += expf(lr[i] - mx);
+    for (int i = tid; i < VOC / 4; i += 256) {
+        float4 v = lr4[i];
+        se += expf(v.x - mx) + expf(v.y - mx) + expf(v.z - mx) + expf(v.w - mx);
+    }
     se = wave_sum(se);
     if (lane == 0) red[w] = se;
     __syncthreads();
     if (tid == 0) {
         float lse = mx + logf(red[0] + red[1] + red[2] + red[3]);
-        lrow[row] = lse - lr[tgt[row]];
+        lrow[row] = lse - logits[(size_t)row * VOC + tgt[row]];
     }
 }
 
@@ -980,9 +999,19 @@
     const size_t need_bytes = (size_t)((char*)(part + (size_t)SKN * TOTCAP * CDIM) - (char*)d_ws);
     const bool use_sk = ws_size >= need_bytes;
 
+    unsigned short* hbufh = (unsigned short*)hbuf;
+    unsigned short* hbufl = hbufh + (size_t)NTOK * CDIM;
     unsigned short* qkvh = (unsigned short*)qkv;
     unsigned short* qkvl = qkvh + (size_t)NTOK * QKVLD;
-    unsigned short* xg_bf  = (unsigned short*)xg;
+    float*          h2   = qkv;
+    unsigned short* h2h  = (unsigned short*)(qkv + (size_t)NTOK * CDIM);
+    unsigned short* h2l  = h2h + (size_t)NTOK * CDIM;
+    float*          ybuf = qkv;
+    unsigned short* xgh  = (unsigned short*)xg;
+    unsigned short* xgl  = xgh + (size_t)TOTCAP * CDIM;
+    unsigned short* xg_bf = (unsigned short*)xg;
+    unsigned short* hidh = (unsigned short*)hid;
+    unsigned short* hidl = hidh + (size_t)TOTCAP * FF;
     unsigned short* hid_bf = (unsigned short*)hid;
     unsigned short* lmw_bf = (unsigned short*)hid;
 
@@ -993,21 +1022,23 @@
     embed_kernel<<<(NTOK * CDIM) / 256, blk, 0, stream>>>(idx, tok_emb, pos_emb, x);
 
     for (int l = 0; l < LCNT; ++l) {
-        ln_kernel<<<NTOK, blk, 0, stream>>>(x, ln1_s + (size_t)l * CDIM, ln1_b + (size_t)l * CDIM, hbuf);
-
-        gemm_splitpb_kernel<0, true><<<dim3(QKVLD / BN, NTOK / BM), blk, 0, stream>>>(
-            CDIM, hbuf, CDIM, wph + (size_t)l * 3 * CDIM * CDIM, wpl + (size_t)l * 3 * CDIM * CDIM,
-            CDIM, nullptr, nullptr, qkvh, qkvl, QKVLD);
-
-        attn_mfma_kernel<<<dim3(TT / QBLK, BB * HCNT), blk, 0, stream>>>(qkvh, qkvl, hbuf);
-
-        gemm_splitpb_kernel<1, false><<<dim3(CDIM / BN, NTOK / BM), blk, 0, stream>>>(
-            CDIM, hbuf, CDIM, woh + (size_t)l * CDIM * CDIM, wol + (size_t)l * CDIM * CDIM,
-            CDIM, bo + (size_t)l * CDIM, x, nullptr, nullptr, CDIM);
-
-        float* h2 = qkv;
-        float* ybuf = qkv;
-        ln_kernel<<<NTOK, blk, 0, stream>>>(x, ln2_s + (size_t)l * CDIM, ln2_b + (size_t)l * CDIM, h2);
+        ln_kernel<false><<<NTOK, blk, 0, stream>>>(
+            x, ln1_s + (size_t)l * CDIM, ln1_b + (size_t)l * CDIM, nullptr, hbufh, hbufl);
+
+        gemm_ps_kernel<0, true><<<dim3(QKVLD / BN, NTOK / BM), blk, 0, stream>>>(
+            CDIM, hbufh, hbufl, CDIM,
+            wph + (size_t)l * 3 * CDIM * CDIM, wpl + (size_t)l * 3 * CDIM * CDIM, CDIM,
+            nullptr, nullptr, qkvh, qkvl, QKVLD);
+
+        attn_mfma_kernel<<<dim3(TT / QBLK, BB * HCNT), blk, 0, stream>>>(qkvh, qkvl, hbufh, hbufl);
+
+        gemm_ps_kernel<1, false><<<dim3(CDIM / BN, NTOK / BM), blk, 0, stream>>>(
+            CDIM, hbufh, hbufl, CDIM,
+            woh + (size_t)l * CDIM * CDIM, wol + (size_t)l * CDIM * CDIM, CDIM,
+            bo + (size_t)l * CDIM, x, nullptr, nullptr, CDIM);
+
+        ln_kernel<true><<<NTOK, blk, 0, stream>>>(
+            x, ln2_s + (size_t)l * CDIM, ln2_b + (size_t)l * CDIM, h2, h2h, h2l);
         gate_kernel<<<NTOK / 256, blk, 0, stream>>>(h2, gate_w + (size_t)l * ECNT * CDIM, sel, wts);
         route_kernel<<<1, blk, 0, stream>>>(sel, perm, tokpos, meta);
 
@@ -1016,23 +1047,25 @@
         const float* w2l = w2 + (size_t)l * ECNT * CDIM * FF;
         const float* b2l = b2 + (size_t)l * ECNT * CDIM;
         if (l == 0) {
-            gather_kernel<<<(TOTCAP * CDIM) / 256, blk, 0, stream>>>(h2, perm, xg);
-            gemm_bf16_kernel<2, true><<<dim3(FF / BN, TOTCAP / BM, ECNT), blk, 0, stream>>>(
-                CDIM, xg, CDIM, w1l, CDIM, b1l, hid, FF, meta, (size_t)FF * CDIM, FF);
+            gather_ps_kernel<<<(TOTCAP * CDIM) / 256, blk, 0, stream>>>(h2h, h2l, perm, xgh, xgl);
+            gemm_pse_kernel<<<dim3(FF / BN, TOTCAP / BM, ECNT), blk, 0, stream>>>(
+                CDIM, xgh, xgl, CDIM, w1l, CDIM, b1l, hidh, hidl, FF,
+                meta, (size_t)FF * CDIM, FF);
             if (use_sk) {
-                gemm_sk_kernel<<<dim3(CDIM / BN, TOTCAP / BM, ECNT * SKN), blk, 0, stream>>>(
-                    FF / SKN, hid, FF, w2l, FF, b2l, part, CDIM, (size_t)TOTCAP * CDIM,
+                gemm_pssk_kernel<SKN><<<dim3(CDIM / BN, TOTCAP / BM, ECNT * SKN), blk, 0, stream>>>(
+                    FF / SKN, hidh, hidl, FF, w2l, FF, b2l, part, CDIM, (size_t)TOTCAP * CDIM,
                     meta, (size_t)CDIM * FF, CDIM);
                 combine_kernel<SKN><<<(NTOK * CDIM) / 256, blk, 0, stream>>>(
                     part, (size_t)TOTCAP * CDIM, tokpos, wts, x);
             } else {
-                gemm_bf16_kernel<0, true><<<dim3(CDIM / BN, TOTCAP / BM, ECNT), blk, 0, stream>>>(
-                    FF, hid, FF, w2l, FF, b2l, ybuf, CDIM, meta, (size_t)CDIM * FF, CDIM);
+                gemm_pssk_kernel<1><<<dim3(CDIM / BN, TOTCAP / BM, ECNT), blk, 0, stream>>>(
+                    FF, hidh, hidl, FF, w2l, FF, b2l, ybuf, CDIM, 0,
+                    meta, (size_t)CDIM * FF, CDIM);
                 combine_kernel<1><<<(NTOK * CDIM) / 256, blk, 0, stream>>>(
                     ybuf, 0, tokpos, wts, x);
             }
         } else {
-            gather_bf16_kernel<<<(TOTCAP * CDIM) / 256, blk, 0, stream>>>(h2, perm, xg_bf);
+            gather_cp_kernel<<<(TOTCAP * CDIM) / 256, blk, 0, stream>>>(h2h, perm, xg_bf);
             gemm_fastw_kernel<2, false, true, false><<<dim3(FF / BN, TOTCAP / BM, ECNT), blk, 0, stream>>>(
                 CDIM, xg_bf, CDIM, w1l, CDIM, b1l, hid_bf, FF, meta, (size_t)FF * CDIM, FF);
             gemm_fastw_kernel<0, false, false, false><<<dim3(CDIM / BN, TOTCAP / BM, ECNT), blk, 0, stream>>>(
```

After: 1.329 ms. 3.1% less time.
